# Optimization experiments

Hardware: AMD Instinct MI355X
Metric: run time of the kernel (lower is better)

Reference implementation:

```python
import jax, jax.numpy as jnp
import numpy as np

NEG_INF_DIAG = 1000000.0

def setup_inputs() -> dict:
    key = jax.random.key(0)
    k1, k2, k3 = jax.random.split(key, 3)
    B, N, S, D = 64, 32, 256, 128
    return {
        "query_embeddings": jax.random.normal(k1, (B, N, D), dtype=jnp.float32),
        "doc_embeddings": jax.random.normal(k2, (B, S, D), dtype=jnp.float32),
        "neg_doc_embeddings": jax.random.normal(k3, (B, S, D), dtype=jnp.float32),
    }

def _maxsim(q, d):
    # q: (b, n, dim), d: (b, s, dim) -> (b,) sum over n of max over s of q.d
    return jnp.einsum('bnd,bsd->bns', q, d).max(axis=2).sum(axis=1)

def reference(query_embeddings, doc_embeddings, neg_doc_embeddings):
    pos_scores = _maxsim(query_embeddings, doc_embeddings)
    neg_scores = _maxsim(query_embeddings, neg_doc_embeddings)
    loss = jax.nn.softplus(neg_scores - pos_scores).mean()

    # in-batch term: scores[b, c] = MaxSim(query b, doc c)
    scores = jnp.einsum('bnd,csd->bcns', query_embeddings, doc_embeddings).max(axis=3).sum(axis=2)  # (B, B)
    pos = jnp.diagonal(scores)
    B = scores.shape[0]
    neg = (scores - jnp.eye(B, dtype=scores.dtype) * NEG_INF_DIAG).max(axis=1)
    loss = loss + jax.nn.softplus(neg - pos).mean()
    return loss / 2
```

## Files before the change

kernel.cpp:

```cpp
#include <hip/hip_runtime.h>
#include <hip/hip_bf16.h>

#define B_SZ 64

typedef __attribute__((ext_vector_type(8))) short bf16x8;
typedef __attribute__((ext_vector_type(4))) float f32x4;

static __device__ __forceinline__ unsigned short f2bf(float f) {
    __hip_bfloat16 h = __float2bfloat16(f);
    return *reinterpret_cast<unsigned short*>(&h);
}

static __device__ __forceinline__ bf16x8 cvt_frag(const float* __restrict__ src) {
    float4 a = reinterpret_cast<const float4*>(src)[0];
    float4 b = reinterpret_cast<const float4*>(src)[1];
    union { bf16x8 v; unsigned short u[8]; } t;
    t.u[0] = f2bf(a.x); t.u[1] = f2bf(a.y); t.u[2] = f2bf(a.z); t.u[3] = f2bf(a.w);
    t.u[4] = f2bf(b.x); t.u[5] = f2bf(b.y); t.u[6] = f2bf(b.z); t.u[7] = f2bf(b.w);
    return t.v;
}

#define MFMA(A, Bv, C) __builtin_amdgcn_mfma_f32_16x16x32_bf16(A, Bv, C, 0, 0, 0)

__global__ __launch_bounds__(256) void cvt_permute(const float* __restrict__ q,
                                                   const float* __restrict__ dd,
                                                   const float* __restrict__ nd,
                                                   unsigned short* __restrict__ DP,
                                                   unsigned short* __restrict__ QP) {
    const int blk = blockIdx.x, tid = threadIdx.x;
    if (blk < 2048) {
        const int o = blk * 256 + tid;
        const int doc = o >> 12;
        const int u = o & 4095;
        const int ln = u & 63, nt = (u >> 6) & 3, kk = (u >> 8) & 3, ch = u >> 10;
        const int s  = ch * 64 + nt * 16 + (ln & 15);
        const int k0 = kk * 32 + (ln >> 4) * 8;
        const float* src = ((doc < 64) ? (dd + (size_t)doc * 32768)
                                       : (nd + (size_t)(doc - 64) * 32768)) + s * 128 + k0;
        reinterpret_cast<bf16x8*>(DP)[o] = cvt_frag(src);
    } else {
        const int g = (blk - 2048) * 256 + tid;
        const int b = g >> 9, u = g & 511;
        const int ln = u & 63, mt = (u >> 6) & 1, kk = u >> 7;
        const int n  = mt * 16 + (ln & 15);
        const int k0 = kk * 32 + (ln >> 4) * 8;
        reinterpret_cast<bf16x8*>(QP)[g] = cvt_frag(q + (size_t)b * 4096 + n * 128 + k0);
    }
}

__global__ __launch_bounds__(256, 3) void maxsim_kernel(const unsigned short* __restrict__ QP,
                                                        const unsigned short* __restrict__ DP,
                                                        float* __restrict__ scores) {
    const int idx = blockIdx.x, tid = threadIdx.x;
    const int wave = tid >> 6, lane = tid & 63;

    __shared__ bf16x8 docB[2048];

    int b0, b1, ccol, dcc;
    const bool isNeg = (idx >= 512);
    if (!isNeg) {
        const int c = idx >> 3, bg = idx & 7;
        b0 = bg * 8 + wave * 2; b1 = b0 + 1;
        ccol = c; dcc = c;
    } else {
        b0 = b1 = idx - 512;
        ccol = B_SZ; dcc = 64 + b0;
    }

    const bf16x8* QP8 = reinterpret_cast<const bf16x8*>(QP);
    const bf16x8* DP8 = reinterpret_cast<const bf16x8*>(DP);

    bf16x8 Af[2][4][2];
    {
        const bf16x8* q0 = QP8 + (size_t)b0 * 512 + lane;
        const bf16x8* q1 = QP8 + (size_t)b1 * 512 + lane;
        #pragma unroll
        for (int kk = 0; kk < 4; ++kk) {
            Af[0][kk][0] = q0[kk * 128];
            Af[0][kk][1] = q0[kk * 128 + 64];
            Af[1][kk][0] = q1[kk * 128];
            Af[1][kk][1] = q1[kk * 128 + 64];
        }
    }

    float rmax[2][2][4];
    #pragma unroll
    for (int qi = 0; qi < 2; ++qi)
        #pragma unroll
        for (int mt = 0; mt < 2; ++mt)
            #pragma unroll
            for (int r = 0; r < 4; ++r) rmax[qi][mt][r] = -3.0e38f;

    const bf16x8* dbase = DP8 + (size_t)dcc * 4096;

    #pragma unroll
    for (int h = 0; h < 2; ++h) {
        if (h) __syncthreads();
        {
            const bf16x8* src = dbase + h * 2048;
            #pragma unroll
            for (int f = 0; f < 8; ++f)
                docB[f * 256 + tid] = src[f * 256 + tid];
        }
        __syncthreads();

        #pragma unroll
        for (int cc = 0; cc < 2; ++cc) {
            f32x4 acc[2][2][4] = {};
            #pragma unroll
            for (int kk = 0; kk < 4; ++kk) {
                #pragma unroll
                for (int nt = 0; nt < 4; ++nt) {
                    bf16x8 Bv = docB[cc * 1024 + kk * 256 + nt * 64 + lane];
                    acc[0][0][nt] = MFMA(Af[0][kk][0], Bv, acc[0][0][nt]);
                    acc[0][1][nt] = MFMA(Af[0][kk][1], Bv, acc[0][1][nt]);
                    acc[1][0][nt] = MFMA(Af[1][kk][0], Bv, acc[1][0][nt]);
                    acc[1][1][nt] = MFMA(Af[1][kk][1], Bv, acc[1][1][nt]);
                }
            }
            #pragma unroll
            for (int qi = 0; qi < 2; ++qi)
                #pragma unroll
                for (int mt = 0; mt < 2; ++mt)
                    #pragma unroll
                    for (int r = 0; r < 4; ++r)
                        rmax[qi][mt][r] = fmaxf(rmax[qi][mt][r],
                            fmaxf(fmaxf(acc[qi][mt][0][r], acc[qi][mt][1][r]),
                                  fmaxf(acc[qi][mt][2][r], acc[qi][mt][3][r])));
        }
    }

    #pragma unroll
    for (int qi = 0; qi < 2; ++qi) {
        float part = 0.0f;
        #pragma unroll
        for (int mt = 0; mt < 2; ++mt)
            #pragma unroll
            for (int r = 0; r < 4; ++r) {
                float m = rmax[qi][mt][r];
                m = fmaxf(m, __shfl_xor(m, 1, 64));
                m = fmaxf(m, __shfl_xor(m, 2, 64));
                m = fmaxf(m, __shfl_xor(m, 4, 64));
                m = fmaxf(m, __shfl_xor(m, 8, 64));
                part += m;
            }
        part += __shfl_xor(part, 16, 64);
        part += __shfl_xor(part, 32, 64);
        const int b = qi ? b1 : b0;
        if (lane == 0 && (!isNeg || (wave == 0 && qi == 0)))
            scores[(size_t)b * 65 + ccol] = part;
    }
}

static __device__ __forceinline__ float softplusf(float x) {
    return fmaxf(x, 0.0f) + log1pf(expf(-fabsf(x)));
}

__global__ __launch_bounds__(64) void loss_kernel(const float* __restrict__ scores,
                                                  float* __restrict__ out) {
    const int b = threadIdx.x;
    const float* row = scores + b * 65;
    const float pos  = row[b];
    const float negq = row[64];
    float nib = -1e30f;
    #pragma unroll
    for (int c = 0; c < B_SZ; ++c) {
        float v = row[c] - ((c == b) ? 1000000.0f : 0.0f);
        nib = fmaxf(nib, v);
    }
    float t = softplusf(negq - pos) + softplusf(nib - pos);
    t += __shfl_xor(t, 1, 64);
    t += __shfl_xor(t, 2, 64);
    t += __shfl_xor(t, 4, 64);
    t += __shfl_xor(t, 8, 64);
    t += __shfl_xor(t, 16, 64);
    t += __shfl_xor(t, 32, 64);
    if (b == 0) out[0] = t * (0.5f / 64.0f);
}

extern "C" void kernel_launch(void* const* d_in, const int* in_sizes, int n_in,
                              void* d_out, int out_size, void* d_ws, size_t ws_size,
                              hipStream_t stream) {
    const float* q  = (const float*)d_in[0];
    const float* dd = (const float*)d_in[1];
    const float* nd = (const float*)d_in[2];
    float* out = (float*)d_out;

    unsigned short* DP = (unsigned short*)d_ws;
    unsigned short* QP = DP + (size_t)128 * 32768;
    float* scores = (float*)(QP + (size_t)64 * 4096);

    cvt_permute<<<2176, 256, 0, stream>>>(q, dd, nd, DP, QP);

    maxsim_kernel<<<512 + B_SZ, 256, 0, stream>>>(QP, DP, scores);

    loss_kernel<<<1, 64, 0, stream>>>(scores, out);
}
```

Measured before the change: 91.57 us.

## Fuse loss into maxsim via last-block atomic and load whole doc into LDS

Removes the separate loss kernel launch: each maxsim block increments a global counter (reset in the conversion kernel), and the last block computes the softplus loss from the scores table. The doc tile is now staged into LDS in a single pass (64KB) instead of two halves with an extra barrier, and each wave starts on a different chunk, presumably to spread LDS bank traffic. The larger LDS footprint lowers the launch-bounds occupancy hint from 3 to 2 blocks per CU, and the added atomic and fences put a small serial tail on the end of the maxsim kernel.

```diff
diff --git a/kernel.cpp b/kernel.cpp
--- a/kernel.cpp
+++ b/kernel.cpp
@@ -22,12 +22,18 @@
 
 #define MFMA(A, Bv, C) __builtin_amdgcn_mfma_f32_16x16x32_bf16(A, Bv, C, 0, 0, 0)
 
+static __device__ __forceinline__ float softplusf(float x) {
+    return fmaxf(x, 0.0f) + log1pf(expf(-fabsf(x)));
+}
+
 __global__ __launch_bounds__(256) void cvt_permute(const float* __restrict__ q,
                                                    const float* __restrict__ dd,
                                                    const float* __restrict__ nd,
                                                    unsigned short* __restrict__ DP,
-                                                   unsigned short* __restrict__ QP) {
+                                                   unsigned short* __restrict__ QP,
+                                                   unsigned int* __restrict__ ctr) {
     const int blk = blockIdx.x, tid = threadIdx.x;
+    if (blk == 0 && tid == 0) *ctr = 0;
     if (blk < 2048) {
         const int o = blk * 256 + tid;
         const int doc = o >> 12;
@@ -48,13 +54,16 @@
     }
 }
 
-__global__ __launch_bounds__(256, 3) void maxsim_kernel(const unsigned short* __restrict__ QP,
+__global__ __launch_bounds__(256, 2) void maxsim_kernel(const unsigned short* __restrict__ QP,
                                                         const unsigned short* __restrict__ DP,
-                                                        float* __restrict__ scores) {
+                                                        float* __restrict__ scores,
+                                                        unsigned int* __restrict__ ctr,
+                                                        float* __restrict__ out) {
     const int idx = blockIdx.x, tid = threadIdx.x;
     const int wave = tid >> 6, lane = tid & 63;
 
-    __shared__ bf16x8 docB[2048];
+    __shared__ bf16x8 docB[4096];
+    __shared__ int lastFlag;
 
     int b0, b1, ccol, dcc;
     const bool isNeg = (idx >= 512);
@@ -83,6 +92,14 @@
         }
     }
 
+    {
+        const bf16x8* src = DP8 + (size_t)dcc * 4096;
+        #pragma unroll
+        for (int f = 0; f < 16; ++f)
+            docB[f * 256 + tid] = src[f * 256 + tid];
+    }
+    __syncthreads();
+
     float rmax[2][2][4];
     #pragma unroll
     for (int qi = 0; qi < 2; ++qi)
@@ -91,43 +108,30 @@
             #pragma unroll
             for (int r = 0; r < 4; ++r) rmax[qi][mt][r] = -3.0e38f;
 
-    const bf16x8* dbase = DP8 + (size_t)dcc * 4096;
-
     #pragma unroll
-    for (int h = 0; h < 2; ++h) {
-        if (h) __syncthreads();
-        {
-            const bf16x8* src = dbase + h * 2048;
-            #pragma unroll
-            for (int f = 0; f < 8; ++f)
-                docB[f * 256 + tid] = src[f * 256 + tid];
+    for (int i = 0; i < 4; ++i) {
+        const int ch = (wave + i) & 3;
+        f32x4 acc[2][2][4] = {};
+        #pragma unroll
+        for (int kk = 0; kk < 4; ++kk) {
+            #pragma unroll
+            for (int nt = 0; nt < 4; ++nt) {
+                bf16x8 Bv = docB[ch * 1024 + kk * 256 + nt * 64 + lane];
+                acc[0][0][nt] = MFMA(Af[0][kk][0], Bv, acc[0][0][nt]);
+                acc[0][1][nt] = MFMA(Af[0][kk][1], Bv, acc[0][1][nt]);
+                acc[1][0][nt] = MFMA(Af[1][kk][0], Bv, acc[1][0][nt]);
+                acc[1][1][nt] = MFMA(Af[1][kk][1], Bv, acc[1][1][nt]);
+            }
         }
-        __syncthreads();
-
-        #pragma unroll
-        for (int cc = 0; cc < 2; ++cc) {
-            f32x4 acc[2][2][4] = {};
-            #pragma unroll
-            for (int kk = 0; kk < 4; ++kk) {
+        #pragma unroll
+        for (int qi = 0; qi < 2; ++qi)
+            #pragma unroll
+            for (int mt = 0; mt < 2; ++mt)
                 #pragma unroll
-                for (int nt = 0; nt < 4; ++nt) {
-                    bf16x8 Bv = docB[cc * 1024 + kk * 256 + nt * 64 + lane];
-                    acc[0][0][nt] = MFMA(Af[0][kk][0], Bv, acc[0][0][nt]);
-                    acc[0][1][nt] = MFMA(Af[0][kk][1], Bv, acc[0][1][nt]);
-                    acc[1][0][nt] = MFMA(Af[1][kk][0], Bv, acc[1][0][nt]);
-                    acc[1][1][nt] = MFMA(Af[1][kk][1], Bv, acc[1][1][nt]);
-                }
-            }
-            #pragma unroll
-            for (int qi = 0; qi < 2; ++qi)
-                #pragma unroll
-                for (int mt = 0; mt < 2; ++mt)
-                    #pragma unroll
-                    for (int r = 0; r < 4; ++r)
-                        rmax[qi][mt][r] = fmaxf(rmax[qi][mt][r],
-                            fmaxf(fmaxf(acc[qi][mt][0][r], acc[qi][mt][1][r]),
-                                  fmaxf(acc[qi][mt][2][r], acc[qi][mt][3][r])));
-        }
+                for (int r = 0; r < 4; ++r)
+                    rmax[qi][mt][r] = fmaxf(rmax[qi][mt][r],
+                        fmaxf(fmaxf(acc[qi][mt][0][r], acc[qi][mt][1][r]),
+                              fmaxf(acc[qi][mt][2][r], acc[qi][mt][3][r])));
     }
 
     #pragma unroll
@@ -150,32 +154,34 @@
         if (lane == 0 && (!isNeg || (wave == 0 && qi == 0)))
             scores[(size_t)b * 65 + ccol] = part;
     }
-}
-
-static __device__ __forceinline__ float softplusf(float x) {
-    return fmaxf(x, 0.0f) + log1pf(expf(-fabsf(x)));
-}
-
-__global__ __launch_bounds__(64) void loss_kernel(const float* __restrict__ scores,
-                                                  float* __restrict__ out) {
-    const int b = threadIdx.x;
-    const float* row = scores + b * 65;
-    const float pos  = row[b];
-    const float negq = row[64];
-    float nib = -1e30f;
-    #pragma unroll
-    for (int c = 0; c < B_SZ; ++c) {
-        float v = row[c] - ((c == b) ? 1000000.0f : 0.0f);
-        nib = fmaxf(nib, v);
-    }
-    float t = softplusf(negq - pos) + softplusf(nib - pos);
-    t += __shfl_xor(t, 1, 64);
-    t += __shfl_xor(t, 2, 64);
-    t += __shfl_xor(t, 4, 64);
-    t += __shfl_xor(t, 8, 64);
-    t += __shfl_xor(t, 16, 64);
-    t += __shfl_xor(t, 32, 64);
-    if (b == 0) out[0] = t * (0.5f / 64.0f);
+
+    __syncthreads();
+    if (tid == 0) {
+        __threadfence();
+        lastFlag = (atomicAdd(ctr, 1u) == 575u);
+    }
+    __syncthreads();
+    if (lastFlag && tid < 64) {
+        __threadfence();
+        const int b = tid;
+        const float* row = scores + b * 65;
+        const float pos  = row[b];
+        const float negq = row[64];
+        float nib = -1e30f;
+        #pragma unroll
+        for (int c = 0; c < B_SZ; ++c) {
+            float v = row[c] - ((c == b) ? 1000000.0f : 0.0f);
+            nib = fmaxf(nib, v);
+        }
+        float t = softplusf(negq - pos) + softplusf(nib - pos);
+        t += __shfl_xor(t, 1, 64);
+        t += __shfl_xor(t, 2, 64);
+        t += __shfl_xor(t, 4, 64);
+        t += __shfl_xor(t, 8, 64);
+        t += __shfl_xor(t, 16, 64);
+        t += __shfl_xor(t, 32, 64);
+        if (b == 0) out[0] = t * (0.5f / 64.0f);
+    }
 }
 
 extern "C" void kernel_launch(void* const* d_in, const int* in_sizes, int n_in,
@@ -189,10 +195,9 @@
     unsigned short* DP = (unsigned short*)d_ws;
     unsigned short* QP = DP + (size_t)128 * 32768;
     float* scores = (float*)(QP + (size_t)64 * 4096);
-
-    cvt_permute<<<2176, 256, 0, stream>>>(q, dd, nd, DP, QP);
-
-    maxsim_kernel<<<512 + B_SZ, 256, 0, stream>>>(QP, DP, scores);
-
-    loss_kernel<<<1, 64, 0, stream>>>(scores, out);
-}
+    unsigned int* ctr = (unsigned int*)(scores + 64 * 65);
+
+    cvt_permute<<<2176, 256, 0, stream>>>(q, dd, nd, DP, QP, ctr);
+
+    maxsim_kernel<<<512 + B_SZ, 256, 0, stream>>>(QP, DP, scores, ctr, out);
+}
```

After: 104.9 us. +14.5%, slower.
